# Kernel tuning notes

Measured on AMD Instinct MI355X. Metric: run time of the kernel, lower is better.

The kernel has to match this reference:

```python
import jax, jax.numpy as jnp
import numpy as np
from jax import lax

HIDDEN = 7168
Q_LORA = 1536
N_HEAD = 64
HEAD_DIM = 128
ROPE_DIM = 64
TOPK = 2048
T = 4096
ROPE_BASE = 10000.0
LN_EPS = 1e-6
NEG_INF = -1e30


def _apply_rope_interleaved(x, cos, sin):
    # x: [..., ROPE_DIM], cos/sin broadcastable to [..., ROPE_DIM//2]
    x1 = x[..., 0::2]
    x2 = x[..., 1::2]
    o1 = x1 * cos - x2 * sin
    o2 = x1 * sin + x2 * cos
    out = jnp.stack([o1, o2], axis=-1)  # interleave back
    return out.reshape(x.shape)


def setup_inputs() -> dict:
    key = jax.random.key(0)
    ks = jax.random.split(key, 6)
    hidden_states = jax.random.normal(ks[0], (T, HIDDEN), dtype=jnp.float32)
    qr = jax.random.normal(ks[1], (T, Q_LORA), dtype=jnp.float32)
    positions = jnp.arange(T, dtype=jnp.int32)
    # learned parameters (stored [in, out] so fwd is x @ W)
    Wq_b = jax.random.normal(ks[2], (Q_LORA, N_HEAD * HEAD_DIM), dtype=jnp.float32) * 0.02
    Wk = jax.random.normal(ks[3], (HIDDEN, HEAD_DIM), dtype=jnp.float32) * 0.02
    Wproj = jax.random.normal(ks[4], (HIDDEN, N_HEAD), dtype=jnp.float32) * 0.02
    k_norm_gamma = jnp.ones((HEAD_DIM,), dtype=jnp.float32)
    k_norm_beta = jnp.zeros((HEAD_DIM,), dtype=jnp.float32)
    return {
        'hidden_states': hidden_states,
        'qr': qr,
        'positions': positions,
        'Wq_b': Wq_b,
        'Wk': Wk,
        'Wproj': Wproj,
        'k_norm_gamma': k_norm_gamma,
        'k_norm_beta': k_norm_beta,
    }


def _indexer_forward(hidden_states, qr, positions, Wq_b, Wk, Wproj, gamma, beta):
    # q projection: [T, n_head * head_dim] -> [T, H, D]
    q = (qr @ Wq_b).reshape(T, N_HEAD, HEAD_DIM)
    q_pe, q_nope = q[..., :ROPE_DIM], q[..., ROPE_DIM:]

    # k projection + LayerNorm (eps=1e-6)
    k = hidden_states @ Wk  # [T, D]
    mu = jnp.mean(k, axis=-1, keepdims=True)
    var = jnp.mean(jnp.square(k - mu), axis=-1, keepdims=True)
    k = (k - mu) * lax.rsqrt(var + LN_EPS) * gamma + beta
    k_pe, k_nope = k[..., :ROPE_DIM], k[..., ROPE_DIM:]

    # RoPE (interleaved / GPT-J style, as used by DeepSeek rotary)
    inv_freq = 1.0 / (ROPE_BASE ** (jnp.arange(0, ROPE_DIM, 2, dtype=jnp.float32) / ROPE_DIM))
    ang = positions.astype(jnp.float32)[:, None] * inv_freq[None, :]  # [T, R/2]
    cos, sin = jnp.cos(ang), jnp.sin(ang)
    q_pe = _apply_rope_interleaved(q_pe, cos[:, None, :], sin[:, None, :])  # [T, H, R]
    k_pe = _apply_rope_interleaved(k_pe, cos, sin)  # [T, R]

    q_full = jnp.concatenate([q_pe, q_nope], axis=-1)  # [T, H, D]
    k_full = jnp.concatenate([k_pe, k_nope], axis=-1)  # [T, D]

    # per-token per-head weights, scaled by head_dim**-0.5 * n_head**-0.5
    w = (hidden_states @ Wproj) * (HEAD_DIM ** -0.5) * (N_HEAD ** -0.5)  # [T, H]

    # lightning-indexer score: sum_h w[t,h] * relu(q[t,h,:] . k[s,:])
    # scan over heads so live intermediate is a single [T, T] matrix
    qh_all = jnp.transpose(q_full, (1, 0, 2))  # [H, T, D]
    wh_all = w.T  # [H, T]

    def body(acc, hw):
        qh, wh = hw  # [T, D], [T]
        acc = acc + wh[:, None] * jax.nn.relu(qh @ k_full.T)
        return acc, None

    scores, _ = lax.scan(body, jnp.zeros((T, T), dtype=jnp.float32), (qh_all, wh_all))

    # causal mask over key positions, then select top-k keys per query
    causal = positions[:, None] >= positions[None, :]
    masked = jnp.where(causal, scores, NEG_INF)
    topk_vals, topk_idx = lax.top_k(masked, TOPK)  # [T, TOPK]
    return topk_vals, topk_idx


def reference(hidden_states, qr, positions, Wq_b, Wk, Wproj, k_norm_gamma, k_norm_beta):
    return _indexer_forward(hidden_states, qr, positions, Wq_b, Wk, Wproj, k_norm_gamma, k_norm_beta)
```

## Files before the change

### kernel.cpp

```cpp
#include <hip/hip_runtime.h>
#include <stdint.h>

#define TT 4096
#define HID 7168
#define QL 1536
#define NH 64
#define HD 128
#define QD 8192
#define KTOP 2048
#define WSCALE 0.011048543456039806f

typedef _Float16 f16;
typedef uint16_t u16;
typedef unsigned u32;
typedef __attribute__((ext_vector_type(4))) float f32x4;
typedef __attribute__((ext_vector_type(16))) float f32x16;
typedef __attribute__((ext_vector_type(8))) _Float16 f16x8;
typedef __attribute__((ext_vector_type(4))) _Float16 f16x4;

__device__ __forceinline__ void lds_load16(const void* g, void* l) {
  __builtin_amdgcn_global_load_lds(
      (const __attribute__((address_space(1))) unsigned*)g,
      (__attribute__((address_space(3))) unsigned*)l, 16, 0, 0);
}

__device__ __forceinline__ u16 f16_bits(f16 h) {
  union { f16 h; u16 u; } c; c.h = h; return c.u;
}
__device__ __forceinline__ float f16_from_bits(u16 u) {
  union { u16 u; f16 h; } c; c.u = u; return (float)c.h;
}

__device__ __forceinline__ size_t soff(int t) {
  int b = t >> 7, r = t & 127;
  return (size_t)128u * ((size_t)(b + 1) * (size_t)(64 * b + r));
}

__global__ void cvt_qr(const float* __restrict__ in, f16* __restrict__ out) {
  int i = blockIdx.x * 256 + threadIdx.x;
  const float4* p = (const float4*)in + (size_t)i * 2;
  float4 a = p[0], b = p[1];
  f16x8 h = {(f16)a.x, (f16)a.y, (f16)a.z, (f16)a.w,
             (f16)b.x, (f16)b.y, (f16)b.z, (f16)b.w};
  *(f16x8*)(out + (size_t)i * 8) = h;
}

__global__ void tcvt(const float* __restrict__ in, f16* __restrict__ out,
                     int R, int C, int ostride, int orow0, int icol0) {
  __shared__ float tile[32][33];
  int cb = blockIdx.x * 32, rb = blockIdx.y * 32;
  int tx = threadIdx.x & 31, ty = threadIdx.x >> 5;
  for (int i = 0; i < 32; i += 8)
    tile[ty + i][tx] = in[(size_t)(rb + ty + i) * C + icol0 + cb + tx];
  __syncthreads();
  for (int i = 0; i < 32; i += 8)
    out[(size_t)(cb + ty + i + orow0) * ostride + rb + tx] = (f16)tile[tx][ty + i];
}

__launch_bounds__(256, 2)
__global__ void gemm_q2(const f16* __restrict__ A, const f16* __restrict__ B,
                        f16* __restrict__ C, int col0) {
  __shared__ __align__(16) f16 As[128 * 32];
  __shared__ __align__(16) f16 Bs[128 * 32];
  int tid = threadIdx.x, lane = tid & 63, wave = tid >> 6;
  int bm = blockIdx.y << 7, bn = blockIdx.x << 7;
  int wm = (wave & 1) << 6, wn = (wave >> 1) << 6;
  int sr = tid >> 2, sc = (tid & 3) * 8;
  const f16* ga = A + (size_t)(bm + sr) * QL + sc;
  const f16* gb = B + (size_t)(bn + sr) * QL + sc;
  f16* la = As + tid * 8;
  f16* lb = Bs + tid * 8;
  f32x4 acc[4][4] = {};
  for (int k0 = 0; k0 < QL; k0 += 32) {
    __syncthreads();
    lds_load16(ga + k0, la);
    lds_load16(ga + (size_t)64 * QL + k0, la + 2048);
    lds_load16(gb + k0, lb);
    lds_load16(gb + (size_t)64 * QL + k0, lb + 2048);
    __syncthreads();
    int ro = lane & 15, ko = (lane >> 4) << 3;
    f16x8 af[4], bf[4];
#pragma unroll
    for (int i = 0; i < 4; i++) af[i] = *(const f16x8*)(As + (wm + i * 16 + ro) * 32 + ko);
#pragma unroll
    for (int i = 0; i < 4; i++) bf[i] = *(const f16x8*)(Bs + (wn + i * 16 + ro) * 32 + ko);
#pragma unroll
    for (int mi = 0; mi < 4; mi++)
#pragma unroll
      for (int ni = 0; ni < 4; ni++)
        acc[mi][ni] = __builtin_amdgcn_mfma_f32_16x16x32_f16(af[mi], bf[ni], acc[mi][ni], 0, 0, 0);
  }
  int cr = (lane >> 4) << 2, cc = lane & 15;
#pragma unroll
  for (int mi = 0; mi < 4; mi++)
#pragma unroll
    for (int ni = 0; ni < 4; ni++) {
      int row = bm + wm + mi * 16 + cr;
      int col = col0 + bn + wn + ni * 16 + cc;
      f16* cp = C + (size_t)row * QD + col;
#pragma unroll
      for (int r = 0; r < 4; r++) cp[(size_t)r * QD] = (f16)acc[mi][ni][r];
    }
}

__launch_bounds__(256, 2)
__global__ void gemm_kw(const float* __restrict__ A, const f16* __restrict__ B,
                        float* __restrict__ kraw, float* __restrict__ wout) {
  __shared__ __align__(16) f16 As[64 * 64];
  __shared__ __align__(16) f16 Bs[64 * 64];
  int tid = threadIdx.x, lane = tid & 63, wave = tid >> 6;
  int bm = blockIdx.y << 6, bn = blockIdx.x << 6;
  int wm = (wave & 1) << 5, wn = (wave >> 1) << 5;
  const f16* gb = B + (size_t)(bn + (tid >> 3)) * HID + (tid & 7) * 8;
  f16* lB = Bs + wave * 512;
  int ar = tid >> 4, ac = (tid & 15) * 4;
  f32x4 acc[2][2] = {};
  for (int k0 = 0; k0 < HID; k0 += 64) {
    __syncthreads();
#pragma unroll
    for (int i = 0; i < 4; i++) {
      float4 v = *(const float4*)(A + (size_t)(bm + ar + i * 16) * HID + k0 + ac);
      f16x4 h = {(f16)v.x, (f16)v.y, (f16)v.z, (f16)v.w};
      *(f16x4*)(As + (ar + i * 16) * 64 + ac) = h;
    }
    lds_load16(gb + k0, lB);
    lds_load16(gb + (size_t)32 * HID + k0, lB + 2048);
    __syncthreads();
    int ro = lane & 15, ko = (lane >> 4) << 3;
    f16x8 af[2][2], bf[2][2];
#pragma unroll
    for (int i = 0; i < 2; i++)
#pragma unroll
      for (int kk = 0; kk < 2; kk++) {
        af[i][kk] = *(const f16x8*)(As + (wm + i * 16 + ro) * 64 + kk * 32 + ko);
        bf[i][kk] = *(const f16x8*)(Bs + (wn + i * 16 + ro) * 64 + kk * 32 + ko);
      }
#pragma unroll
    for (int mi = 0; mi < 2; mi++)
#pragma unroll
      for (int ni = 0; ni < 2; ni++)
#pragma unroll
        for (int kk = 0; kk < 2; kk++)
          acc[mi][ni] = __builtin_amdgcn_mfma_f32_16x16x32_f16(af[mi][kk], bf[ni][kk], acc[mi][ni], 0, 0, 0);
  }
  int cr = (lane >> 4) << 2, cc = lane & 15;
#pragma unroll
  for (int mi = 0; mi < 2; mi++)
#pragma unroll
    for (int ni = 0; ni < 2; ni++) {
      int row = bm + wm + mi * 16 + cr;
      int col = bn + wn + ni * 16 + cc;
#pragma unroll
      for (int r = 0; r < 4; r++) {
        float v = acc[mi][ni][r];
        int rr = row + r;
        if (col < HD) kraw[(size_t)rr * HD + col] = v;
        else          wout[(size_t)rr * NH + (col - HD)] = v * WSCALE;
      }
    }
}

__global__ void ln_rope(const float* __restrict__ kraw, const int* __restrict__ pos,
                        const float* __restrict__ gamma, const float* __restrict__ beta,
                        f16* __restrict__ k16) {
  int row = (blockIdx.x << 2) + (threadIdx.x >> 6);
  int lane = threadIdx.x & 63;
  const float* kr = kraw + (size_t)row * HD;
  float2 x = ((const float2*)kr)[lane];
  float s = x.x + x.y, s2 = x.x * x.x + x.y * x.y;
  for (int off = 32; off; off >>= 1) { s += __shfl_down(s, off); s2 += __shfl_down(s2, off); }
  s = __shfl(s, 0); s2 = __shfl(s2, 0);
  float mu = s * (1.f / 128.f);
  float var = s2 * (1.f / 128.f) - mu * mu;
  float inv = rsqrtf(var + 1e-6f);
  float y0 = (x.x - mu) * inv * gamma[lane * 2] + beta[lane * 2];
  float y1 = (x.y - mu) * inv * gamma[lane * 2 + 1] + beta[lane * 2 + 1];
  float o0 = y0, o1 = y1;
  if (lane < 32) {
    float p = (float)pos[row];
    float invf = exp2f(-(float)lane * 0.41524101185942813f);
    float ang = p * invf;
    float sn, cn;
    sincosf(ang, &sn, &cn);
    o0 = y0 * cn - y1 * sn;
    o1 = y0 * sn + y1 * cn;
  }
  k16[(size_t)row * HD + 2 * lane] = (f16)o0;
  k16[(size_t)row * HD + 2 * lane + 1] = (f16)o1;
}

__global__ void rope_q(f16* __restrict__ q16, const int* __restrict__ pos) {
  int t = blockIdx.x, tid = threadIdx.x;
  __shared__ float cs[64];
  if (tid < 32) {
    float invf = exp2f(-(float)tid * 0.41524101185942813f);
    float ang = (float)pos[t] * invf;
    float sn, cn;
    sincosf(ang, &sn, &cn);
    cs[tid] = cn;
    cs[32 + tid] = sn;
  }
  __syncthreads();
  f16* row = q16 + (size_t)t * QD;
#pragma unroll
  for (int it = 0; it < 2; it++) {
    int u = it * 256 + tid;
    int h = u >> 3, c = u & 7;
    f16* p = row + h * HD + c * 8;
    f16x8 v = *(f16x8*)p;
#pragma unroll
    for (int j = 0; j < 4; j++) {
      int l = c * 4 + j;
      float cn = cs[l], sn = cs[32 + l];
      float x = (float)v[2 * j], y = (float)v[2 * j + 1];
      v[2 * j] = (f16)(x * cn - y * sn);
      v[2 * j + 1] = (f16)(x * sn + y * cn);
    }
    *(f16x8*)p = v;
  }
}

__launch_bounds__(256, 3)
__global__ void scores2(const f16* __restrict__ q16, const f16* __restrict__ k16,
                        const float* __restrict__ w, f16* __restrict__ S) {
  int bid = (int)blockIdx.x;
  bid = (bid & 7) * 136 + (bid >> 3);
  int g = 0;
  while (4 * (g + 1) * (g + 2) <= bid) g++;
  int rem = bid - 4 * g * (g + 1);
  int qt = (g << 3) + rem / (g + 1);
  int kt = rem - (rem / (g + 1)) * (g + 1);
  int kt0 = kt << 8, qt0 = qt << 5;

  int tid = threadIdx.x, l = tid & 63, wid = tid >> 6;
  int q = l & 31, half = l >> 5;
  __shared__ __align__(16) f16 smem_q[4 * 4096];
  __shared__ float w_lds[2048];

  for (int i = tid; i < 2048; i += 256) {
    int hh = i & 63, qq = i >> 6;
    w_lds[hh * 32 + qq] = w[(size_t)(qt0 + qq) * NH + hh];
  }
  f16x8 kfr[2][8];
  {
    const f16* kb = k16 + (size_t)(kt0 + wid * 64 + q) * HD + half * 8;
#pragma unroll
    for (int mt = 0; mt < 2; mt++)
#pragma unroll
      for (int kk = 0; kk < 8; kk++)
        kfr[mt][kk] = *(const f16x8*)(kb + mt * 32 * HD + kk * 16);
  }
  __syncthreads();
  asm volatile("s_waitcnt vmcnt(0)" ::: "memory");

  const f16* qbase = q16 + (size_t)qt0 * QD;
  auto stage = [&](int h) {
    const f16* src = qbase + h * HD;
    f16* dst = smem_q + (h & 3) * 4096;
#pragma unroll
    for (int p = 0; p < 2; p++) {
      int u = p * 256 + tid;
      lds_load16(src + (size_t)(u & 31) * QD + (u >> 5) * 8, dst + u * 8);
    }
  };

  f32x16 s0 = {}, s1 = {};
  auto compute = [&](int h) {
    const f16* qb = smem_q + (h & 3) * 4096;
    f32x16 a0 = {}, a1 = {};
    __builtin_amdgcn_s_setprio(1);
#pragma unroll
    for (int kk = 0; kk < 8; kk++) {
      f16x8 qf = *(const f16x8*)(qb + ((kk * 2 + half) * 32 + q) * 8);
      a0 = __builtin_amdgcn_mfma_f32_32x32x16_f16(kfr[0][kk], qf, a0, 0, 0, 0);
      a1 = __builtin_amdgcn_mfma_f32_32x32x16_f16(kfr[1][kk], qf, a1, 0, 0, 0);
    }
    __builtin_amdgcn_s_setprio(0);
    float wv = w_lds[h * 32 + q];
#pragma unroll
    for (int r = 0; r < 16; r++) {
      s0[r] += wv * fmaxf(a0[r], 0.f);
      s1[r] += wv * fmaxf(a1[r], 0.f);
    }
  };

  stage(0); stage(1); stage(2);
  for (int h = 0; h < 61; h++) {
    asm volatile("s_waitcnt vmcnt(4)" ::: "memory");
    __builtin_amdgcn_s_barrier();
    asm volatile("" ::: "memory");
    stage(h + 3);
    compute(h);
  }
  asm volatile("s_waitcnt vmcnt(4)" ::: "memory");
  __builtin_amdgcn_s_barrier();
  asm volatile("" ::: "memory");
  compute(61);
  asm volatile("s_waitcnt vmcnt(2)" ::: "memory");
  __builtin_amdgcn_s_barrier();
  asm volatile("" ::: "memory");
  compute(62);
  asm volatile("s_waitcnt vmcnt(0)" ::: "memory");
  __builtin_amdgcn_s_barrier();
  asm volatile("" ::: "memory");
  compute(63);

  f16* st = smem_q;
#pragma unroll
  for (int mt = 0; mt < 2; mt++)
#pragma unroll
    for (int r = 0; r < 16; r++) {
      int m = (r & 3) + ((r >> 2) << 3) + half * 4;
      int sl = wid * 64 + mt * 32 + m;
      float v = mt ? s1[r] : s0[r];
      if (!(v == v)) v = 0.f;
      v = fminf(fmaxf(v, -60000.f), 60000.f);
      u32 byte = (u32)(q * 512 + sl * 2) ^ (u32)((q & 7) << 4);
      *(f16*)((char*)st + byte) = (f16)v;
    }
  __syncthreads();
  {
    int rq = tid >> 3, c = tid & 7;
    int t = qt0 + rq;
    size_t base = soff(t) + (size_t)kt0;
    bool hi = (t - kt0) >= 128;
#pragma unroll
    for (int j = 0; j < 4; j++) {
      if (c < 4 || hi) {
        u32 byte = (u32)(rq * 512 + c * 64 + j * 16) ^ (u32)((rq & 7) << 4);
        uint4 v = *(uint4*)((char*)st + byte);
        *(uint4*)(S + base + c * 32 + j * 8) = v;
      }
    }
  }
}

template <int N>
__device__ __forceinline__ void sort_and_store(u32* key, int tid, int t, float* out) {
  constexpr int V = N / 256;
  u32 v[V];
#pragma unroll
  for (int r = 0; r < V; r += 4) {
    uint4 q4 = *(const uint4*)(key + tid * V + r);
    v[r] = ~q4.x; v[r + 1] = ~q4.y; v[r + 2] = ~q4.z; v[r + 3] = ~q4.w;
  }
#pragma unroll
  for (int k = 2; k <= N; k <<= 1) {
#pragma unroll
    for (int j = k >> 1; j > 0; j >>= 1) {
      if (j >= 64 * V) {
#pragma unroll
        for (int r = 0; r < V; r += 4) {
          uint4 q4 = {v[r], v[r + 1], v[r + 2], v[r + 3]};
          *(uint4*)(key + tid * V + r) = q4;
        }
        __syncthreads();
        for (int m = tid; m < N / 2; m += 256) {
          int i = ((m & ~(j - 1)) << 1) | (m & (j - 1));
          int l = i | j;
          bool up = ((i & k) == 0);
          u32 a = key[i], b = key[l];
          if (up ? (a > b) : (a < b)) { key[i] = b; key[l] = a; }
        }
        __syncthreads();
#pragma unroll
        for (int r = 0; r < V; r += 4) {
          uint4 q4 = *(const uint4*)(key + tid * V + r);
          v[r] = q4.x; v[r + 1] = q4.y; v[r + 2] = q4.z; v[r + 3] = q4.w;
        }
      } else if (j >= V) {
        int lanej = j / V;
        bool takeMin = (((tid & lanej) == 0) == (((tid * V) & k) == 0));
#pragma unroll
        for (int r = 0; r < V; r++) {
          u32 o = __shfl_xor(v[r], lanej, 64);
          u32 mn = min(v[r], o), mx = max(v[r], o);
          v[r] = takeMin ? mn : mx;
        }
      } else {
#pragma unroll
        for (int r = 0; r < V; r++) {
          if ((r & j) == 0) {
            bool up = (((tid * V + r) & k) == 0);
            u32 a = v[r], b = v[r | j];
            u32 mn = min(a, b), mx = max(a, b);
            v[r] = up ? mn : mx;
            v[r | j] = up ? mx : mn;
          }
        }
      }
    }
  }
  if (tid * V < KTOP) {
    float* ov = out + (size_t)t * KTOP + tid * V;
    float* oi = out + (size_t)TT * KTOP + (size_t)t * KTOP + tid * V;
#pragma unroll
    for (int r = 0; r < V; r++) {
      u32 kv = ~v[r];
      u32 mono = kv >> 16;
      float val;
      if (mono == 0u) {
        val = -1e30f;
      } else {
        u16 hb = (u16)((mono & 0x8000u) ? (mono ^ 0x8000u) : (mono ^ 0xFFFFu));
        val = f16_from_bits(hb);
      }
      ov[r] = val;
      oi[r] = (float)(0xFFFFu - (kv & 0xFFFFu));
    }
  }
}

__launch_bounds__(256, 4)
__global__ void topk_k(const f16* __restrict__ S, float* __restrict__ out) {
  int t = blockIdx.x, tid = threadIdx.x;
  __shared__ __align__(16) u32 key[4096];
  size_t base = soff(t);
  int nsort = (t <= 2047) ? 2048 : 4096;
  const uint4* src = (const uint4*)(S + base);
  for (int i = tid; i < (nsort >> 3); i += 256) {
    uint4 v4 = src[i];
    u32 ww[4] = {v4.x, v4.y, v4.z, v4.w};
#pragma unroll
    for (int j = 0; j < 8; j++) {
      int s = i * 8 + j;
      u32 kk;
      if (s > t) {
        kk = 0xFFFFu - (u32)s;
      } else {
        u16 hb = (u16)(ww[j >> 1] >> ((j & 1) * 16));
        u32 mono = (hb & 0x8000u) ? (u32)(hb ^ 0xFFFFu) : (u32)(hb | 0x8000u);
        kk = (mono << 16) | (0xFFFFu - (u32)s);
      }
      key[s] = kk;
    }
  }
  __syncthreads();
  if (t <= 2047) sort_and_store<2048>(key, tid, t, out);
  else           sort_and_store<4096>(key, tid, t, out);
}

extern "C" void kernel_launch(void* const* d_in, const int* in_sizes, int n_in,
                              void* d_out, int out_size, void* d_ws, size_t ws_size,
                              hipStream_t stream) {
  const float* hs = (const float*)d_in[0];
  const float* qr = (const float*)d_in[1];
  const int* pos = (const int*)d_in[2];
  const float* Wq = (const float*)d_in[3];
  const float* Wk = (const float*)d_in[4];
  const float* Wp = (const float*)d_in[5];
  const float* gamma = (const float*)d_in[6];
  const float* beta = (const float*)d_in[7];
  char* ws = (char*)d_ws;
  f16* qr16 = (f16*)ws;
  f16* wqTh = (f16*)(ws + 12582912);
  float* kraw = (float*)ws;
  float* wsc = (float*)(ws + 2097152);
  f16* k16 = (f16*)(ws + 3145728);
  f16* kwT = (f16*)(ws + 4194304);
  f16* S = (f16*)(ws + 4194304);
  f16* q16 = (f16*)(ws + 32112640);

  cvt_qr<<<dim3(3072), dim3(256), 0, stream>>>(qr, qr16);
  tcvt<<<dim3(128, 48), dim3(256), 0, stream>>>(Wq, wqTh, QL, QD, QL, 0, 0);
  gemm_q2<<<dim3(32, 32), dim3(256), 0, stream>>>(qr16, wqTh, q16, 0);
  tcvt<<<dim3(128, 48), dim3(256), 0, stream>>>(Wq, wqTh, QL, QD, QL, 0, 4096);
  gemm_q2<<<dim3(32, 32), dim3(256), 0, stream>>>(qr16, wqTh, q16, 4096);
  rope_q<<<dim3(4096), dim3(256), 0, stream>>>(q16, pos);
  tcvt<<<dim3(4, 224), dim3(256), 0, stream>>>(Wk, kwT, HID, HD, HID, 0, 0);
  tcvt<<<dim3(2, 224), dim3(256), 0, stream>>>(Wp, kwT, HID, NH, HID, HD, 0);
  gemm_kw<<<dim3(3, 64), dim3(256), 0, stream>>>(hs, kwT, kraw, wsc);
  ln_rope<<<dim3(1024), dim3(256), 0, stream>>>(kraw, pos, gamma, beta, k16);
  scores2<<<dim3(1088), dim3(256), 0, stream>>>(q16, k16, wsc, S);
  topk_k<<<dim3(4096), dim3(256), 0, stream>>>(S, (float*)d_out);
}
```

Measured before the change: 802.9 us.

## Swizzle LDS layouts in GEMMs, widen q-GEMM K tile, use DPP/swizzle in bitonic

Result: faster. 776.3 us (-3.3%).

```diff
diff --git a/kernel.cpp b/kernel.cpp
--- a/kernel.cpp
+++ b/kernel.cpp
@@ -29,6 +29,15 @@
 }
 __device__ __forceinline__ float f16_from_bits(u16 u) {
   union { u16 u; f16 h; } c; c.u = u; return (float)c.h;
+}
+
+__device__ __forceinline__ u32 xlane(u32 x, int lj) {
+  if (lj == 1)  return (u32)__builtin_amdgcn_mov_dpp((int)x, 0xB1, 0xF, 0xF, true);
+  if (lj == 2)  return (u32)__builtin_amdgcn_mov_dpp((int)x, 0x4E, 0xF, 0xF, true);
+  if (lj == 4)  return (u32)__builtin_amdgcn_ds_swizzle((int)x, 0x101F);
+  if (lj == 8)  return (u32)__builtin_amdgcn_ds_swizzle((int)x, 0x201F);
+  if (lj == 16) return (u32)__builtin_amdgcn_ds_swizzle((int)x, 0x401F);
+  return (u32)__shfl_xor((int)x, lj, 64);
 }
 
 __device__ __forceinline__ size_t soff(int t) {
@@ -60,35 +69,43 @@
 __launch_bounds__(256, 2)
 __global__ void gemm_q2(const f16* __restrict__ A, const f16* __restrict__ B,
                         f16* __restrict__ C, int col0) {
-  __shared__ __align__(16) f16 As[128 * 32];
-  __shared__ __align__(16) f16 Bs[128 * 32];
+  __shared__ __align__(16) f16 As[128 * 64];
+  __shared__ __align__(16) f16 Bs[128 * 64];
   int tid = threadIdx.x, lane = tid & 63, wave = tid >> 6;
   int bm = blockIdx.y << 7, bn = blockIdx.x << 7;
   int wm = (wave & 1) << 6, wn = (wave >> 1) << 6;
-  int sr = tid >> 2, sc = (tid & 3) * 8;
-  const f16* ga = A + (size_t)(bm + sr) * QL + sc;
-  const f16* gb = B + (size_t)(bn + sr) * QL + sc;
+  int srow = tid >> 3;
+  int sc8 = (tid & 7) ^ (srow & 7);
+  const f16* ga = A + (size_t)(bm + srow) * QL + sc8 * 8;
+  const f16* gb = B + (size_t)(bn + srow) * QL + sc8 * 8;
   f16* la = As + tid * 8;
   f16* lb = Bs + tid * 8;
   f32x4 acc[4][4] = {};
-  for (int k0 = 0; k0 < QL; k0 += 32) {
+  for (int k0 = 0; k0 < QL; k0 += 64) {
     __syncthreads();
-    lds_load16(ga + k0, la);
-    lds_load16(ga + (size_t)64 * QL + k0, la + 2048);
-    lds_load16(gb + k0, lb);
-    lds_load16(gb + (size_t)64 * QL + k0, lb + 2048);
+#pragma unroll
+    for (int p = 0; p < 4; p++) {
+      lds_load16(ga + (size_t)(p * 32) * QL + k0, la + p * 2048);
+      lds_load16(gb + (size_t)(p * 32) * QL + k0, lb + p * 2048);
+    }
     __syncthreads();
-    int ro = lane & 15, ko = (lane >> 4) << 3;
-    f16x8 af[4], bf[4];
-#pragma unroll
-    for (int i = 0; i < 4; i++) af[i] = *(const f16x8*)(As + (wm + i * 16 + ro) * 32 + ko);
-#pragma unroll
-    for (int i = 0; i < 4; i++) bf[i] = *(const f16x8*)(Bs + (wn + i * 16 + ro) * 32 + ko);
-#pragma unroll
-    for (int mi = 0; mi < 4; mi++)
-#pragma unroll
-      for (int ni = 0; ni < 4; ni++)
-        acc[mi][ni] = __builtin_amdgcn_mfma_f32_16x16x32_f16(af[mi], bf[ni], acc[mi][ni], 0, 0, 0);
+    int ro = lane & 15, kg = lane >> 4;
+    f16x8 af[4][2], bf[4][2];
+#pragma unroll
+    for (int i = 0; i < 4; i++)
+#pragma unroll
+      for (int kk = 0; kk < 2; kk++) {
+        int c8 = (kk * 4 + kg) ^ (ro & 7);
+        af[i][kk] = *(const f16x8*)(As + (wm + i * 16 + ro) * 64 + c8 * 8);
+        bf[i][kk] = *(const f16x8*)(Bs + (wn + i * 16 + ro) * 64 + c8 * 8);
+      }
+#pragma unroll
+    for (int kk = 0; kk < 2; kk++)
+#pragma unroll
+      for (int mi = 0; mi < 4; mi++)
+#pragma unroll
+        for (int ni = 0; ni < 4; ni++)
+          acc[mi][ni] = __builtin_amdgcn_mfma_f32_16x16x32_f16(af[mi][kk], bf[ni][kk], acc[mi][ni], 0, 0, 0);
   }
   int cr = (lane >> 4) << 2, cc = lane & 15;
 #pragma unroll
@@ -111,9 +128,12 @@
   int tid = threadIdx.x, lane = tid & 63, wave = tid >> 6;
   int bm = blockIdx.y << 6, bn = blockIdx.x << 6;
   int wm = (wave & 1) << 5, wn = (wave >> 1) << 5;
-  const f16* gb = B + (size_t)(bn + (tid >> 3)) * HID + (tid & 7) * 8;
+  int srow = tid >> 3;
+  int sc8 = (tid & 7) ^ (srow & 7);
+  const f16* gb = B + (size_t)(bn + srow) * HID + sc8 * 8;
   f16* lB = Bs + wave * 512;
   int ar = tid >> 4, ac = (tid & 15) * 4;
+  int awc8 = (ac >> 3), awsub = ac & 7;
   f32x4 acc[2][2] = {};
   for (int k0 = 0; k0 < HID; k0 += 64) {
     __syncthreads();
@@ -121,19 +141,21 @@
     for (int i = 0; i < 4; i++) {
       float4 v = *(const float4*)(A + (size_t)(bm + ar + i * 16) * HID + k0 + ac);
       f16x4 h = {(f16)v.x, (f16)v.y, (f16)v.z, (f16)v.w};
-      *(f16x4*)(As + (ar + i * 16) * 64 + ac) = h;
+      int row = ar + i * 16;
+      *(f16x4*)(As + row * 64 + (awc8 ^ (row & 7)) * 8 + awsub) = h;
     }
     lds_load16(gb + k0, lB);
     lds_load16(gb + (size_t)32 * HID + k0, lB + 2048);
     __syncthreads();
-    int ro = lane & 15, ko = (lane >> 4) << 3;
+    int ro = lane & 15, kg = lane >> 4;
     f16x8 af[2][2], bf[2][2];
 #pragma unroll
     for (int i = 0; i < 2; i++)
 #pragma unroll
       for (int kk = 0; kk < 2; kk++) {
-        af[i][kk] = *(const f16x8*)(As + (wm + i * 16 + ro) * 64 + kk * 32 + ko);
-        bf[i][kk] = *(const f16x8*)(Bs + (wn + i * 16 + ro) * 64 + kk * 32 + ko);
+        int c8 = (kk * 4 + kg) ^ (ro & 7);
+        af[i][kk] = *(const f16x8*)(As + (wm + i * 16 + ro) * 64 + c8 * 8);
+        bf[i][kk] = *(const f16x8*)(Bs + (wn + i * 16 + ro) * 64 + c8 * 8);
       }
 #pragma unroll
     for (int mi = 0; mi < 2; mi++)
@@ -373,7 +395,7 @@
         bool takeMin = (((tid & lanej) == 0) == (((tid * V) & k) == 0));
 #pragma unroll
         for (int r = 0; r < V; r++) {
-          u32 o = __shfl_xor(v[r], lanej, 64);
+          u32 o = xlane(v[r], lanej);
           u32 mn = min(v[r], o), mx = max(v[r], o);
           v[r] = takeMin ? mn : mx;
         }
```
